# Optimization experiments

Hardware: AMD Instinct MI355X
Metric: run time of the kernel (lower is better)

## Reference

```python
import jax, jax.numpy as jnp
import numpy as np

EPS = 1e-6


def setup_inputs() -> dict:
    key = jax.random.key(0)
    ks = jax.random.split(key, 7)
    T, B, D, N = 512, 32, 1024, 128
    scale_w = (6.0 / (N + D)) ** 0.5  # xavier_uniform bound
    def w(k):
        return jax.random.uniform(k, (N, D), jnp.float32, -scale_w, scale_w)
    return {
        "x": jax.random.normal(ks[0], (T, B, D), jnp.float32),
        "S0": jnp.zeros((B, N, N), jnp.float32),
        "W_k": w(ks[1]),
        "W_v": w(ks[2]),
        "W_q": w(ks[3]),
        "W_erase": w(ks[4]),
        "W_write": w(ks[5]),
    }


def _ntm_forward(x, S0, W_k, W_v, W_q, W_erase, W_write):
    # Projections for all timesteps at once: (T, B, n_state)
    k = jnp.einsum('tbd,nd->tbn', x, W_k)
    v = jnp.einsum('tbd,nd->tbn', x, W_v)
    q = jnp.einsum('tbd,nd->tbn', x, W_q)
    erase = jnp.einsum('tbd,nd->tbn', x, W_erase)  # use_sigmoid=False: raw
    write = jnp.einsum('tbd,nd->tbn', x, W_write)

    def step(S, inp):
        k_t, v_t, q_t, e_t, w_t = inp
        k_norm = k_t / (jnp.linalg.norm(k_t, axis=-1, keepdims=True) + EPS)
        # S: (B, n, n); outer products via broadcasting
        erase_outer = e_t[:, :, None] * k_norm[:, None, :]
        write_outer = (w_t * v_t)[:, :, None] * k_norm[:, None, :]
        S_new = jnp.tanh(S * (1.0 - erase_outer) + write_outer)
        Sq = jnp.einsum('bij,bj->bi', S_new, q_t)
        out = Sq * jax.nn.silu(Sq)
        return S_new, out

    S_final, outputs = jax.lax.scan(step, S0, (k, v, q, erase, write))
    return outputs, S_final


def reference(x, S0, W_k, W_v, W_q, W_erase, W_write):
    return _ntm_forward(x, S0, W_k, W_v, W_q, W_erase, W_write)
```

## Files before the change

kernel.cpp:

```cpp
#include <hip/hip_runtime.h>
#include <hip/hip_bf16.h>


typedef __attribute__((ext_vector_type(8))) short bf16x8;
typedef __attribute__((ext_vector_type(4))) float f32x4;
typedef __attribute__((ext_vector_type(2))) float f32x2;
typedef __attribute__((ext_vector_type(4))) unsigned short u16x4;
typedef __attribute__((ext_vector_type(8))) unsigned short u16x8;

static constexpr int T_STEPS = 512;
static constexpr int BATCH   = 32;
static constexpr int DDIM    = 1024;
static constexpr int NDIM    = 128;
static constexpr int LDC     = 5 * NDIM;
static constexpr int MROWS   = T_STEPS * BATCH;
static constexpr int OUT_N   = T_STEPS * BATCH * NDIM;

static constexpr size_t C_BYTES  = (size_t)MROWS * LDC * 4;
static constexpr size_t W2_BYTES = 5ull * NDIM * DDIM * 2;

__device__ __forceinline__ unsigned short rne_bf16(float v) {
    unsigned u = __builtin_bit_cast(unsigned, v);
    u += 0x7FFFu + ((u >> 16) & 1u);
    return (unsigned short)(u >> 16);
}

__global__ __launch_bounds__(256) void wconv_kernel(
    const float* __restrict__ w0, const float* __restrict__ w1,
    const float* __restrict__ w2, const float* __restrict__ w3,
    const float* __restrict__ w4,
    unsigned short* __restrict__ W2)
{
    const int idx = blockIdx.x * 256 + threadIdx.x;
    const size_t e = (size_t)idx * 4;
    const int bn = (int)(e >> 17);
    const int r  = (int)(e & 131071);
    const int n  = r >> 10;
    const int k  = r & 1023;

    const float* wp = w0;
    if (bn == 1) wp = w1;
    else if (bn == 2) wp = w2;
    else if (bn == 3) wp = w3;
    else if (bn == 4) wp = w4;

    f32x4 v = *(const f32x4*)(wp + r);
    u16x4 h;
#pragma unroll
    for (int j = 0; j < 4; ++j) h[j] = rne_bf16(v[j]);

    const int kk   = k >> 5;
    const int quad = (k >> 3) & 3;
    const size_t off = ((((size_t)(bn * 32 + kk) * 128 + n) * 4 + quad) * 8) + (k & 7);
    *(u16x4*)(W2 + off) = h;
}

template<int BN0, int NB>
__device__ __forceinline__ void gemm_pass(
    const unsigned short (&lds)[64 * 1024],
    const unsigned short* __restrict__ bp,
    float* __restrict__ C,
    int m0, int wave, int quad, int l16, int aswz)
{
    auto LDA = [&](int mi, int kk) -> bf16x8 {
        const int byteo = (mi * 16 + l16) * 2048 + ((kk * 64 + quad * 16) ^ aswz);
        return *(const bf16x8*)((const char*)lds + byteo);
    };

    f32x4 acc[NB][4];
#pragma unroll
    for (int q = 0; q < NB; ++q)
#pragma unroll
        for (int mi = 0; mi < 4; ++mi) acc[q][mi] = (f32x4)(0.0f);

    const unsigned short* bpp[NB];
#pragma unroll
    for (int q = 0; q < NB; ++q) bpp[q] = bp + (size_t)(BN0 + q) * 131072;

    bf16x8 aC[4], bC[NB], aN[4], bN[NB];
#pragma unroll
    for (int mi = 0; mi < 4; ++mi) aC[mi] = LDA(mi, 0);
#pragma unroll
    for (int q = 0; q < NB; ++q) bC[q] = *(const bf16x8*)bpp[q];

    for (int kk = 0; kk < 32; kk += 2) {
#pragma unroll
        for (int mi = 0; mi < 4; ++mi) aN[mi] = LDA(mi, kk + 1);
#pragma unroll
        for (int q = 0; q < NB; ++q)
            bN[q] = *(const bf16x8*)(bpp[q] + (size_t)(kk + 1) * 4096);
#pragma unroll
        for (int q = 0; q < NB; ++q)
#pragma unroll
            for (int mi = 0; mi < 4; ++mi)
                acc[q][mi] = __builtin_amdgcn_mfma_f32_16x16x32_bf16(
                    aC[mi], bC[q], acc[q][mi], 0, 0, 0);
        if (kk < 30) {
#pragma unroll
            for (int mi = 0; mi < 4; ++mi) aC[mi] = LDA(mi, kk + 2);
#pragma unroll
            for (int q = 0; q < NB; ++q)
                bC[q] = *(const bf16x8*)(bpp[q] + (size_t)(kk + 2) * 4096);
        }
#pragma unroll
        for (int q = 0; q < NB; ++q)
#pragma unroll
            for (int mi = 0; mi < 4; ++mi)
                acc[q][mi] = __builtin_amdgcn_mfma_f32_16x16x32_bf16(
                    aN[mi], bN[q], acc[q][mi], 0, 0, 0);
    }

#pragma unroll
    for (int q = 0; q < NB; ++q)
#pragma unroll
        for (int mi = 0; mi < 4; ++mi) {
            const int rw = m0 + mi * 16 + quad * 4;
            const int cl = (BN0 + q) * 128 + wave * 16 + l16;
#pragma unroll
            for (int r = 0; r < 4; ++r)
                C[(size_t)(rw + r) * LDC + cl] = acc[q][mi][r];
        }
}

__global__ __launch_bounds__(512, 2) void gemm5_kernel(
    const float* __restrict__ x,
    const unsigned short* __restrict__ W2,
    float* __restrict__ C)
{
    __shared__ unsigned short lds[64 * 1024];

    const int m0   = blockIdx.x * 64;
    const int tid  = threadIdx.x;
    const int wave = tid >> 6, lane = tid & 63;
    const int quad = lane >> 4, l16 = lane & 15;

    {
        const int k8 = tid & 127;
        const int rb = tid >> 7;
#pragma unroll 4
        for (int it = 0; it < 16; ++it) {
            const int row = it * 4 + rb;
            const float* src = x + (size_t)(m0 + row) * DDIM + k8 * 8;
            f32x4 v0 = *(const f32x4*)src;
            f32x4 v1 = *(const f32x4*)(src + 4);
            u16x8 h;
            h[0] = rne_bf16(v0[0]); h[1] = rne_bf16(v0[1]);
            h[2] = rne_bf16(v0[2]); h[3] = rne_bf16(v0[3]);
            h[4] = rne_bf16(v1[0]); h[5] = rne_bf16(v1[1]);
            h[6] = rne_bf16(v1[2]); h[7] = rne_bf16(v1[3]);
            const int byteo = row * 2048 + ((k8 * 16) ^ ((row & 7) << 4));
            *(u16x8*)((char*)lds + byteo) = h;
        }
    }
    __syncthreads();

    const int aswz = (l16 & 7) << 4;
    const unsigned short* bp = W2 + ((size_t)((wave * 16 + l16) * 4 + quad)) * 8;

    gemm_pass<0, 2>(lds, bp, C, m0, wave, quad, l16, aswz);
    gemm_pass<2, 2>(lds, bp, C, m0, wave, quad, l16, aswz);
    gemm_pass<4, 1>(lds, bp, C, m0, wave, quad, l16, aswz);
}

__global__ __launch_bounds__(256) void knorm_kernel(float* __restrict__ C)
{
    const int r    = blockIdx.x * 4 + (threadIdx.x >> 6);
    const int lane = threadIdx.x & 63;
    float* base = C + (size_t)r * LDC;

    f32x2 k2 = *(const f32x2*)(base + lane * 2);
    f32x2 v2 = *(const f32x2*)(base + NDIM + lane * 2);
    f32x2 w2 = *(const f32x2*)(base + 4 * NDIM + lane * 2);

    float ss = k2.x * k2.x + k2.y * k2.y;
#pragma unroll
    for (int off = 32; off >= 1; off >>= 1) ss += __shfl_xor(ss, off, 64);
    float inv = __builtin_amdgcn_rcpf(sqrtf(ss) + 1e-6f);

    f32x2 kn = {k2.x * inv, k2.y * inv};
    f32x2 wv = {v2.x * w2.x, v2.y * w2.y};
    *(f32x2*)(base + lane * 2) = kn;
    *(f32x2*)(base + NDIM + lane * 2) = wv;
}

__device__ __forceinline__ float tanh_fast(float xx) {
    float ex = __builtin_amdgcn_exp2f(xx * 2.8853900817779268f);
    float r  = __builtin_amdgcn_rcpf(ex + 1.0f);
    return fmaf(-2.0f, r, 1.0f);
}

template <int CTRL, int RMASK>
__device__ __forceinline__ float dpp_add(float x) {
    int yi = __builtin_amdgcn_update_dpp(
        0, __builtin_bit_cast(int, x), CTRL, RMASK, 0xF, true);
    return x + __builtin_bit_cast(float, yi);
}

__device__ __forceinline__ float dpp_reduce32(float x) {
    x = dpp_add<0xB1,  0xF>(x);
    x = dpp_add<0x4E,  0xF>(x);
    x = dpp_add<0x141, 0xF>(x);
    x = dpp_add<0x140, 0xF>(x);
    x = dpp_add<0x142, 0xA>(x);
    return x;
}

template<int NOUTER, bool TAIL>
__global__ __launch_bounds__(256, 2) void ntm_scan_part(
    const float* __restrict__ C, const float* __restrict__ Sin,
    float* __restrict__ Sout, float* __restrict__ out, int t0)
{
    const int L    = blockIdx.x;
    const int b    = (L & 7) + 8 * ((L >> 3) & 3);
    const int row  = (L >> 5) * 8 + (threadIdx.x >> 5);
    const int g    = threadIdx.x & 31;
    const int col0 = g * 4;

    f32x4 S = *(const f32x4*)(Sin + ((size_t)b * NDIM + row) * NDIM + col0);

    const size_t STRIDE = (size_t)BATCH * LDC;
    const float* pb = C + (size_t)b * LDC;
    const float* p0 = pb + (size_t)t0 * STRIDE;

    f32x4 kS[4], qS[4];
    float eS[4], wvS[4];

#pragma unroll
    for (int s = 0; s < 2; ++s) {
        const float* p = p0 + (size_t)s * STRIDE;
        kS[s]  = *(const f32x4*)(p + col0);
        qS[s]  = *(const f32x4*)(p + 2 * NDIM + col0);
        eS[s]  = p[3 * NDIM + row];
        wvS[s] = p[NDIM + row];
    }

    float* opc = out + (size_t)t0 * BATCH * NDIM + (size_t)b * NDIM + row;
    const float* pc = p0 + 2 * STRIDE;

    for (int ti = 0; ti < NOUTER; ++ti) {
#pragma unroll
        for (int j = 0; j < 4; ++j) {
            const int ps = (j + 2) & 3;
            kS[ps]  = *(const f32x4*)(pc + col0);
            qS[ps]  = *(const f32x4*)(pc + 2 * NDIM + col0);
            eS[ps]  = pc[3 * NDIM + row];
            wvS[ps] = pc[NDIM + row];
            pc += STRIDE;

            float dot = 0.0f;
#pragma unroll
            for (int u = 0; u < 4; ++u) {
                float t0v = fmaf(-eS[j], S[u], wvS[j]);
                float pre = fmaf(kS[j][u], t0v, S[u]);
                S[u] = tanh_fast(pre);
                dot = fmaf(S[u], qS[j][u], dot);
            }
            dot = dpp_reduce32(dot);

            if ((threadIdx.x & 31) == 31)
                *opc = dot;
            opc += BATCH * NDIM;
        }
    }

    if (TAIL) {
#pragma unroll
        for (int j = 0; j < 4; ++j) {
            const int ps = (j + 2) & 3;
            int tp = t0 + NOUTER * 4 + 2 + j;
            if (tp > T_STEPS - 1) tp = T_STEPS - 1;
            const float* p = pb + (size_t)tp * STRIDE;
            kS[ps]  = *(const f32x4*)(p + col0);
            qS[ps]  = *(const f32x4*)(p + 2 * NDIM + col0);
            eS[ps]  = p[3 * NDIM + row];
            wvS[ps] = p[NDIM + row];

            float dot = 0.0f;
#pragma unroll
            for (int u = 0; u < 4; ++u) {
                float t0v = fmaf(-eS[j], S[u], wvS[j]);
                float pre = fmaf(kS[j][u], t0v, S[u]);
                S[u] = tanh_fast(pre);
                dot = fmaf(S[u], qS[j][u], dot);
            }
            dot = dpp_reduce32(dot);

            if ((threadIdx.x & 31) == 31)
                *opc = dot;
            opc += BATCH * NDIM;
        }
    }

    *(f32x4*)(Sout + ((size_t)b * NDIM + row) * NDIM + col0) = S;
}

__global__ __launch_bounds__(256) void silu_kernel(float* __restrict__ out)
{
    const int i = blockIdx.x * 256 + threadIdx.x;
    f32x4 d = ((const f32x4*)out)[i];
    f32x4 y;
#pragma unroll
    for (int j = 0; j < 4; ++j) {
        float sg = __builtin_amdgcn_rcpf(
            1.0f + __builtin_amdgcn_exp2f(-d[j] * 1.4426950408889634f));
        y[j] = d[j] * d[j] * sg;
    }
    ((f32x4*)out)[i] = y;
}

extern "C" void kernel_launch(void* const* d_in, const int* in_sizes, int n_in,
                              void* d_out, int out_size, void* d_ws, size_t ws_size,
                              hipStream_t stream) {
    const float* x  = (const float*)d_in[0];
    const float* S0 = (const float*)d_in[1];
    const float* wk = (const float*)d_in[2];
    const float* wv = (const float*)d_in[3];
    const float* wq = (const float*)d_in[4];
    const float* we = (const float*)d_in[5];
    const float* ww = (const float*)d_in[6];
    float* out = (float*)d_out;
    float* C   = (float*)d_ws;
    unsigned short* W2 = (unsigned short*)((char*)d_ws + C_BYTES);
    float* S_mid = (float*)((char*)d_ws + C_BYTES + W2_BYTES);

    wconv_kernel<<<640, 256, 0, stream>>>(wk, wv, wq, we, ww, W2);
    gemm5_kernel<<<256, 512, 0, stream>>>(x, W2, C);
    knorm_kernel<<<MROWS / 4, 256, 0, stream>>>(C);
    ntm_scan_part<64, false><<<512, 256, 0, stream>>>(C, S0, S_mid, out, 0);
    ntm_scan_part<63, true><<<512, 256, 0, stream>>>(
        C, S_mid, out + (size_t)OUT_N, out, 256);
    silu_kernel<<<OUT_N / 1024, 256, 0, stream>>>(out);
}
```

Before: 268.1 us.

## Fuse key normalization and write*value into GEMM epilogue, deepen B prefetch

Removes the separate knorm kernel by computing the k row-norm inside the GEMM via a shuffle plus LDS cross-wave reduction, and forming w*v in registers before storing. Passes are regrouped as (v,w), (k,q), (e) so the needed products are available in the epilogue. The inner K loop is also restructured with a 4-deep register prefetch of B operands. This saves a full read/write pass over C and a launch, at the cost of higher register pressure and an extra block barrier.

```diff
diff --git a/kernel.cpp b/kernel.cpp
--- a/kernel.cpp
+++ b/kernel.cpp
@@ -55,79 +55,87 @@
     *(u16x4*)(W2 + off) = h;
 }
 
-template<int BN0, int NB>
-__device__ __forceinline__ void gemm_pass(
-    const unsigned short (&lds)[64 * 1024],
-    const unsigned short* __restrict__ bp,
-    float* __restrict__ C,
-    int m0, int wave, int quad, int l16, int aswz)
+template<int NB>
+__device__ __forceinline__ void run_pass(
+    const unsigned short* __restrict__ ldsb,
+    const unsigned short* const (&bpp)[NB],
+    int l16, int quad, int aswz,
+    f32x4 (&acc)[NB][4])
 {
     auto LDA = [&](int mi, int kk) -> bf16x8 {
+        if (kk > 31) kk = 31;
         const int byteo = (mi * 16 + l16) * 2048 + ((kk * 64 + quad * 16) ^ aswz);
-        return *(const bf16x8*)((const char*)lds + byteo);
+        return *(const bf16x8*)((const char*)ldsb + byteo);
     };
-
-    f32x4 acc[NB][4];
+    auto LDB = [&](int q, int kk) -> bf16x8 {
+        if (kk > 31) kk = 31;
+        return *(const bf16x8*)(bpp[q] + (size_t)kk * 4096);
+    };
+
 #pragma unroll
     for (int q = 0; q < NB; ++q)
 #pragma unroll
         for (int mi = 0; mi < 4; ++mi) acc[q][mi] = (f32x4)(0.0f);
 
-    const unsigned short* bpp[NB];
-#pragma unroll
-    for (int q = 0; q < NB; ++q) bpp[q] = bp + (size_t)(BN0 + q) * 131072;
-
-    bf16x8 aC[4], bC[NB], aN[4], bN[NB];
-#pragma unroll
-    for (int mi = 0; mi < 4; ++mi) aC[mi] = LDA(mi, 0);
-#pragma unroll
-    for (int q = 0; q < NB; ++q) bC[q] = *(const bf16x8*)bpp[q];
-
-    for (int kk = 0; kk < 32; kk += 2) {
-#pragma unroll
-        for (int mi = 0; mi < 4; ++mi) aN[mi] = LDA(mi, kk + 1);
-#pragma unroll
-        for (int q = 0; q < NB; ++q)
-            bN[q] = *(const bf16x8*)(bpp[q] + (size_t)(kk + 1) * 4096);
+    bf16x8 a0[4], a1[4], b0[NB], b1[NB], b2[NB], b3[NB];
+#pragma unroll
+    for (int mi = 0; mi < 4; ++mi) a0[mi] = LDA(mi, 0);
+#pragma unroll
+    for (int q = 0; q < NB; ++q) {
+        b0[q] = LDB(q, 0); b1[q] = LDB(q, 1);
+        b2[q] = LDB(q, 2); b3[q] = LDB(q, 3);
+    }
+
+    for (int kk = 0; kk < 32; kk += 4) {
+#pragma unroll
+        for (int mi = 0; mi < 4; ++mi) a1[mi] = LDA(mi, kk + 1);
 #pragma unroll
         for (int q = 0; q < NB; ++q)
 #pragma unroll
             for (int mi = 0; mi < 4; ++mi)
                 acc[q][mi] = __builtin_amdgcn_mfma_f32_16x16x32_bf16(
-                    aC[mi], bC[q], acc[q][mi], 0, 0, 0);
-        if (kk < 30) {
-#pragma unroll
-            for (int mi = 0; mi < 4; ++mi) aC[mi] = LDA(mi, kk + 2);
-#pragma unroll
-            for (int q = 0; q < NB; ++q)
-                bC[q] = *(const bf16x8*)(bpp[q] + (size_t)(kk + 2) * 4096);
-        }
+                    a0[mi], b0[q], acc[q][mi], 0, 0, 0);
+#pragma unroll
+        for (int q = 0; q < NB; ++q) b0[q] = LDB(q, kk + 4);
+#pragma unroll
+        for (int mi = 0; mi < 4; ++mi) a0[mi] = LDA(mi, kk + 2);
 #pragma unroll
         for (int q = 0; q < NB; ++q)
 #pragma unroll
             for (int mi = 0; mi < 4; ++mi)
                 acc[q][mi] = __builtin_amdgcn_mfma_f32_16x16x32_bf16(
-                    aN[mi], bN[q], acc[q][mi], 0, 0, 0);
-    }
-
-#pragma unroll
-    for (int q = 0; q < NB; ++q)
-#pragma unroll
-        for (int mi = 0; mi < 4; ++mi) {
-            const int rw = m0 + mi * 16 + quad * 4;
-            const int cl = (BN0 + q) * 128 + wave * 16 + l16;
-#pragma unroll
-            for (int r = 0; r < 4; ++r)
-                C[(size_t)(rw + r) * LDC + cl] = acc[q][mi][r];
-        }
-}
-
-__global__ __launch_bounds__(512, 2) void gemm5_kernel(
+                    a1[mi], b1[q], acc[q][mi], 0, 0, 0);
+#pragma unroll
+        for (int q = 0; q < NB; ++q) b1[q] = LDB(q, kk + 5);
+#pragma unroll
+        for (int mi = 0; mi < 4; ++mi) a1[mi] = LDA(mi, kk + 3);
+#pragma unroll
+        for (int q = 0; q < NB; ++q)
+#pragma unroll
+            for (int mi = 0; mi < 4; ++mi)
+                acc[q][mi] = __builtin_amdgcn_mfma_f32_16x16x32_bf16(
+                    a0[mi], b2[q], acc[q][mi], 0, 0, 0);
+#pragma unroll
+        for (int q = 0; q < NB; ++q) b2[q] = LDB(q, kk + 6);
+#pragma unroll
+        for (int mi = 0; mi < 4; ++mi) a0[mi] = LDA(mi, kk + 4);
+#pragma unroll
+        for (int q = 0; q < NB; ++q)
+#pragma unroll
+            for (int mi = 0; mi < 4; ++mi)
+                acc[q][mi] = __builtin_amdgcn_mfma_f32_16x16x32_bf16(
+                    a1[mi], b3[q], acc[q][mi], 0, 0, 0);
+#pragma unroll
+        for (int q = 0; q < NB; ++q) b3[q] = LDB(q, kk + 7);
+    }
+}
+
+__global__ __launch_bounds__(512, 2) void gemm6_kernel(
     const float* __restrict__ x,
     const unsigned short* __restrict__ W2,
     float* __restrict__ C)
 {
-    __shared__ unsigned short lds[64 * 1024];
+    __shared__ unsigned short lds[64 * 1024 + 1024];
 
     const int m0   = blockIdx.x * 64;
     const int tid  = threadIdx.x;
@@ -156,31 +164,74 @@
 
     const int aswz = (l16 & 7) << 4;
     const unsigned short* bp = W2 + ((size_t)((wave * 16 + l16) * 4 + quad)) * 8;
-
-    gemm_pass<0, 2>(lds, bp, C, m0, wave, quad, l16, aswz);
-    gemm_pass<2, 2>(lds, bp, C, m0, wave, quad, l16, aswz);
-    gemm_pass<4, 1>(lds, bp, C, m0, wave, quad, l16, aswz);
-}
-
-__global__ __launch_bounds__(256) void knorm_kernel(float* __restrict__ C)
-{
-    const int r    = blockIdx.x * 4 + (threadIdx.x >> 6);
-    const int lane = threadIdx.x & 63;
-    float* base = C + (size_t)r * LDC;
-
-    f32x2 k2 = *(const f32x2*)(base + lane * 2);
-    f32x2 v2 = *(const f32x2*)(base + NDIM + lane * 2);
-    f32x2 w2 = *(const f32x2*)(base + 4 * NDIM + lane * 2);
-
-    float ss = k2.x * k2.x + k2.y * k2.y;
-#pragma unroll
-    for (int off = 32; off >= 1; off >>= 1) ss += __shfl_xor(ss, off, 64);
-    float inv = __builtin_amdgcn_rcpf(sqrtf(ss) + 1e-6f);
-
-    f32x2 kn = {k2.x * inv, k2.y * inv};
-    f32x2 wv = {v2.x * w2.x, v2.y * w2.y};
-    *(f32x2*)(base + lane * 2) = kn;
-    *(f32x2*)(base + NDIM + lane * 2) = wv;
+    float* lds2f = (float*)((char*)lds + 131072);
+
+    auto STORE = [&](int bn, const f32x4 (&a)[4]) {
+#pragma unroll
+        for (int mi = 0; mi < 4; ++mi) {
+            const int rw = m0 + mi * 16 + quad * 4;
+            const int cl = bn * 128 + wave * 16 + l16;
+#pragma unroll
+            for (int r = 0; r < 4; ++r)
+                C[(size_t)(rw + r) * LDC + cl] = a[mi][r];
+        }
+    };
+
+    f32x4 wv[4];
+    {
+        const unsigned short* bppVW[2] = { bp + 1 * 131072, bp + 4 * 131072 };
+        f32x4 acc[2][4];
+        run_pass<2>(lds, bppVW, l16, quad, aswz, acc);
+#pragma unroll
+        for (int mi = 0; mi < 4; ++mi)
+#pragma unroll
+            for (int r = 0; r < 4; ++r)
+                wv[mi][r] = acc[0][mi][r] * acc[1][mi][r];
+    }
+
+    {
+        const unsigned short* bppKQ[2] = { bp, bp + 2 * 131072 };
+        f32x4 acc[2][4];
+        run_pass<2>(lds, bppKQ, l16, quad, aswz, acc);
+
+#pragma unroll
+        for (int mi = 0; mi < 4; ++mi)
+#pragma unroll
+            for (int r = 0; r < 4; ++r) {
+                float s = acc[0][mi][r] * acc[0][mi][r];
+                s += __shfl_xor(s, 1);
+                s += __shfl_xor(s, 2);
+                s += __shfl_xor(s, 4);
+                s += __shfl_xor(s, 8);
+                if (l16 == 0)
+                    lds2f[(mi * 16 + quad * 4 + r) * 8 + wave] = s;
+            }
+        __syncthreads();
+
+#pragma unroll
+        for (int mi = 0; mi < 4; ++mi)
+#pragma unroll
+            for (int r = 0; r < 4; ++r) {
+                const int row = mi * 16 + quad * 4 + r;
+                f32x4 p0 = *(const f32x4*)&lds2f[row * 8];
+                f32x4 p1 = *(const f32x4*)&lds2f[row * 8 + 4];
+                float ss = (p0[0] + p0[1]) + (p0[2] + p0[3])
+                         + (p1[0] + p1[1]) + (p1[2] + p1[3]);
+                float inv = __builtin_amdgcn_rcpf(sqrtf(ss) + 1e-6f);
+                acc[0][mi][r] *= inv;
+            }
+
+        STORE(0, acc[0]);
+        STORE(1, wv);
+        STORE(2, acc[1]);
+    }
+
+    {
+        const unsigned short* bppE[1] = { bp + 3 * 131072 };
+        f32x4 acc[1][4];
+        run_pass<1>(lds, bppE, l16, quad, aswz, acc);
+        STORE(3, acc[0]);
+    }
 }
 
 __device__ __forceinline__ float tanh_fast(float xx) {
@@ -324,8 +375,7 @@
     float* S_mid = (float*)((char*)d_ws + C_BYTES + W2_BYTES);
 
     wconv_kernel<<<640, 256, 0, stream>>>(wk, wv, wq, we, ww, W2);
-    gemm5_kernel<<<256, 512, 0, stream>>>(x, W2, C);
-    knorm_kernel<<<MROWS / 4, 256, 0, stream>>>(C);
+    gemm6_kernel<<<256, 512, 0, stream>>>(x, W2, C);
     ntm_scan_part<64, false><<<512, 256, 0, stream>>>(C, S0, S_mid, out, 0);
     ntm_scan_part<63, true><<<512, 256, 0, stream>>>(
         C, S_mid, out + (size_t)OUT_N, out, 256);
```

Measured after the change: 275.5 us. 2.7% more time.

## Spread each state row across a full wavefront with two columns per lane

Applied to the files above, without the earlier changes.

The scan kernel now maps one S row to a 64-lane wavefront, with each lane holding 2 columns instead of 4, and adds a sixth DPP step for the full-wave reduction. The grid doubles to 1024 blocks and the launch bounds request 4 blocks per CU. This shortens each thread's serial per-timestep chain and raises parallelism for the latency-bound recurrence. In exchange it adds a reduction step and doubles the redundant per-row loads of e and wv.

```diff
diff --git a/kernel.cpp b/kernel.cpp
--- a/kernel.cpp
+++ b/kernel.cpp
@@ -196,40 +196,41 @@
     return x + __builtin_bit_cast(float, yi);
 }
 
-__device__ __forceinline__ float dpp_reduce32(float x) {
+__device__ __forceinline__ float dpp_reduce64(float x) {
     x = dpp_add<0xB1,  0xF>(x);
     x = dpp_add<0x4E,  0xF>(x);
     x = dpp_add<0x141, 0xF>(x);
     x = dpp_add<0x140, 0xF>(x);
     x = dpp_add<0x142, 0xA>(x);
+    x = dpp_add<0x143, 0xC>(x);
     return x;
 }
 
 template<int NOUTER, bool TAIL>
-__global__ __launch_bounds__(256, 2) void ntm_scan_part(
+__global__ __launch_bounds__(256, 4) void ntm_scan2(
     const float* __restrict__ C, const float* __restrict__ Sin,
     float* __restrict__ Sout, float* __restrict__ out, int t0)
 {
     const int L    = blockIdx.x;
     const int b    = (L & 7) + 8 * ((L >> 3) & 3);
-    const int row  = (L >> 5) * 8 + (threadIdx.x >> 5);
-    const int g    = threadIdx.x & 31;
-    const int col0 = g * 4;
-
-    f32x4 S = *(const f32x4*)(Sin + ((size_t)b * NDIM + row) * NDIM + col0);
+    const int row  = (L >> 5) * 4 + (threadIdx.x >> 6);
+    const int lane = threadIdx.x & 63;
+    const int col0 = lane * 2;
+
+    f32x2 S = *(const f32x2*)(Sin + ((size_t)b * NDIM + row) * NDIM + col0);
 
     const size_t STRIDE = (size_t)BATCH * LDC;
     const float* pb = C + (size_t)b * LDC;
     const float* p0 = pb + (size_t)t0 * STRIDE;
 
-    f32x4 kS[4], qS[4];
+    f32x2 kS[4], qS[4];
     float eS[4], wvS[4];
 
 #pragma unroll
     for (int s = 0; s < 2; ++s) {
         const float* p = p0 + (size_t)s * STRIDE;
-        kS[s]  = *(const f32x4*)(p + col0);
-        qS[s]  = *(const f32x4*)(p + 2 * NDIM + col0);
+        kS[s]  = *(const f32x2*)(p + col0);
+        qS[s]  = *(const f32x2*)(p + 2 * NDIM + col0);
         eS[s]  = p[3 * NDIM + row];
         wvS[s] = p[NDIM + row];
     }
@@ -241,23 +242,23 @@
 #pragma unroll
         for (int j = 0; j < 4; ++j) {
             const int ps = (j + 2) & 3;
-            kS[ps]  = *(const f32x4*)(pc + col0);
-            qS[ps]  = *(const f32x4*)(pc + 2 * NDIM + col0);
+            kS[ps]  = *(const f32x2*)(pc + col0);
+            qS[ps]  = *(const f32x2*)(pc + 2 * NDIM + col0);
             eS[ps]  = pc[3 * NDIM + row];
             wvS[ps] = pc[NDIM + row];
             pc += STRIDE;
 
             float dot = 0.0f;
 #pragma unroll
-            for (int u = 0; u < 4; ++u) {
+            for (int u = 0; u < 2; ++u) {
                 float t0v = fmaf(-eS[j], S[u], wvS[j]);
                 float pre = fmaf(kS[j][u], t0v, S[u]);
                 S[u] = tanh_fast(pre);
                 dot = fmaf(S[u], qS[j][u], dot);
             }
-            dot = dpp_reduce32(dot);
-
-            if ((threadIdx.x & 31) == 31)
+            dot = dpp_reduce64(dot);
+
+            if (lane == 63)
                 *opc = dot;
             opc += BATCH * NDIM;
         }
@@ -270,28 +271,28 @@
             int tp = t0 + NOUTER * 4 + 2 + j;
             if (tp > T_STEPS - 1) tp = T_STEPS - 1;
             const float* p = pb + (size_t)tp * STRIDE;
-            kS[ps]  = *(const f32x4*)(p + col0);
-            qS[ps]  = *(const f32x4*)(p + 2 * NDIM + col0);
+            kS[ps]  = *(const f32x2*)(p + col0);
+            qS[ps]  = *(const f32x2*)(p + 2 * NDIM + col0);
             eS[ps]  = p[3 * NDIM + row];
             wvS[ps] = p[NDIM + row];
 
             float dot = 0.0f;
 #pragma unroll
-            for (int u = 0; u < 4; ++u) {
+            for (int u = 0; u < 2; ++u) {
                 float t0v = fmaf(-eS[j], S[u], wvS[j]);
                 float pre = fmaf(kS[j][u], t0v, S[u]);
                 S[u] = tanh_fast(pre);
                 dot = fmaf(S[u], qS[j][u], dot);
             }
-            dot = dpp_reduce32(dot);
-
-            if ((threadIdx.x & 31) == 31)
+            dot = dpp_reduce64(dot);
+
+            if (lane == 63)
                 *opc = dot;
             opc += BATCH * NDIM;
         }
     }
 
-    *(f32x4*)(Sout + ((size_t)b * NDIM + row) * NDIM + col0) = S;
+    *(f32x2*)(Sout + ((size_t)b * NDIM + row) * NDIM + col0) = S;
 }
 
 __global__ __launch_bounds__(256) void silu_kernel(float* __restrict__ out)
@@ -326,8 +327,8 @@
     wconv_kernel<<<640, 256, 0, stream>>>(wk, wv, wq, we, ww, W2);
     gemm5_kernel<<<256, 512, 0, stream>>>(x, W2, C);
     knorm_kernel<<<MROWS / 4, 256, 0, stream>>>(C);
-    ntm_scan_part<64, false><<<512, 256, 0, stream>>>(C, S0, S_mid, out, 0);
-    ntm_scan_part<63, true><<<512, 256, 0, stream>>>(
+    ntm_scan2<64, false><<<1024, 256, 0, stream>>>(C, S0, S_mid, out, 0);
+    ntm_scan2<63, true><<<1024, 256, 0, stream>>>(
         C, S_mid, out + (size_t)OUT_N, out, 256);
     silu_kernel<<<OUT_N / 1024, 256, 0, stream>>>(out);
 }
```

New measurement: 318.3 us. +18.7%, slower.
